# Kernel optimization log

Measured on AMD Instinct MI355X. Metric: run time of the kernel, lower is better.

The kernel has to match this reference:

```python
import jax, jax.numpy as jnp
import numpy as np

N_NODES = 50000
N_EDGES = 25000
NNZ = 800000
IN_DIM = 256
OUT_DIM = 256


def setup_inputs() -> dict:
    key = jax.random.key(0)
    k1, k2, k3, k4, k5 = jax.random.split(key, 5)
    X = jax.random.normal(k1, (N_NODES, IN_DIM), dtype=jnp.float32)
    node_idx = jax.random.randint(k2, (NNZ,), 0, N_NODES, dtype=jnp.int64)
    edge_idx = jax.random.randint(k3, (NNZ,), 0, N_EDGES, dtype=jnp.int64)
    # Xavier-uniform-ish weight, zero bias (matches reset_parameters)
    limit = float(np.sqrt(6.0 / (IN_DIM + OUT_DIM)))
    W = jax.random.uniform(k4, (IN_DIM, OUT_DIM), dtype=jnp.float32, minval=-limit, maxval=limit)
    b = jnp.zeros((OUT_DIM,), dtype=jnp.float32)
    return {"X": X, "node_idx": node_idx, "edge_idx": edge_idx, "W": W, "b": b}


def reference(X, node_idx, edge_idx, W, b):
    # Y = X @ W + b  -- dense GEMM
    Y = X @ W + b  # [N, out_dim]

    ones = jnp.ones(node_idx.shape[0], dtype=Y.dtype)
    # D_v = rowsum(H)^-0.5 (inf -> 0); D_e = colsum(H)^-1 (inf -> 0)
    deg_v = jax.ops.segment_sum(ones, node_idx, num_segments=N_NODES)
    deg_e = jax.ops.segment_sum(ones, edge_idx, num_segments=N_EDGES)
    d_v = jnp.where(deg_v > 0, deg_v ** -0.5, 0.0)  # [N]
    d_e = jnp.where(deg_e > 0, 1.0 / deg_e, 0.0)    # [E]

    # step1 = H^T @ (D_v X): gather scaled node rows, scatter-add into edges
    Z = d_v[:, None] * Y                                   # [N, out_dim]
    step1 = jax.ops.segment_sum(Z[node_idx], edge_idx, num_segments=N_EDGES)  # [E, out_dim]
    # step2 = D_e @ step1
    step2 = d_e[:, None] * step1                           # [E, out_dim]
    # step3 = H @ step2: gather edge rows, scatter-add into nodes
    step3 = jax.ops.segment_sum(step2[edge_idx], node_idx, num_segments=N_NODES)  # [N, out_dim]
    # final = D_v @ step3
    return d_v[:, None] * step3
```

## Files before the change

kernel.cpp:

```cpp
#include <hip/hip_runtime.h>

#define N_NODES 50000
#define N_EDGES 25000
#define NNZ     800000
#define DIM     256

#define CAP_E 88
#define CAP_V 56

#define NBE 98
#define NBV 196
#define CE_COARSE 8800
#define CV_COARSE 4500
#define NNZ_PB 2048
#define P1_BLOCKS 391

#define B_A1   0
#define B_CE   0
#define B_CV   3449600
#define B_CSRE 12800000
#define B_CSRV 17200000
#define B_WT   22800000
#define B_CURV 22931072
#define B_CURE 23131072
#define B_CCUR 23331072
#define B_DV   23332248

typedef __attribute__((ext_vector_type(8))) short s8v;
typedef __attribute__((ext_vector_type(4))) float f4v;

__device__ __forceinline__ unsigned short f2bf(float f) {
    unsigned u = __float_as_uint(f);
    u = (u + 0x7FFFu + ((u >> 16) & 1u)) >> 16;
    return (unsigned short)u;
}
__device__ __forceinline__ float bf2f(unsigned short h) {
    return __uint_as_float(((unsigned)h) << 16);
}

__global__ __launch_bounds__(256) void k_prep(
        const float* __restrict__ W,
        const int* __restrict__ node_idx, const int* __restrict__ edge_idx,
        unsigned short* __restrict__ WTb,
        unsigned* __restrict__ ccurE, unsigned* __restrict__ ccurV,
        unsigned* __restrict__ coarseE, unsigned* __restrict__ coarseV) {
    if (blockIdx.x < 32) {
        int t = blockIdx.x * 256 + threadIdx.x;
        int n = t >> 5;
        int k0 = (t & 31) * 8;
        unsigned short o[8];
#pragma unroll
        for (int j = 0; j < 8; ++j) o[j] = f2bf(W[(size_t)(k0 + j) * DIM + n]);
        *(s8v*)(WTb + (size_t)n * DIM + k0) = *(const s8v*)o;
        return;
    }

    __shared__ unsigned histE[NBE], histV[NBV], baseE[NBE], baseV[NBV];
    __shared__ unsigned offE[NBE], offV[NBV];
    __shared__ unsigned scanE[256], scanV[256];
    __shared__ unsigned nEs, nVs;
    __shared__ unsigned bufE[NNZ_PB], dstE[NNZ_PB];
    __shared__ unsigned bufV[NNZ_PB], dstV[NNZ_PB];
    const int tid = threadIdx.x;
    const int pb  = blockIdx.x - 32;
    const int base = pb * NNZ_PB;

    if (tid < NBE) histE[tid] = 0;
    if (tid < NBV) histV[tid] = 0;
    __syncthreads();

    int idx0 = base + tid * 4;
    int idx1 = base + 1024 + tid * 4;
    bool ok0 = idx0 < NNZ, ok1 = idx1 < NNZ;
    int4 v0 = ok0 ? *(const int4*)(node_idx + idx0) : (int4){0,0,0,0};
    int4 e0 = ok0 ? *(const int4*)(edge_idx + idx0) : (int4){0,0,0,0};
    int4 v1 = ok1 ? *(const int4*)(node_idx + idx1) : (int4){0,0,0,0};
    int4 e1 = ok1 ? *(const int4*)(edge_idx + idx1) : (int4){0,0,0,0};
    int vv[8] = {v0.x, v0.y, v0.z, v0.w, v1.x, v1.y, v1.z, v1.w};
    int ee[8] = {e0.x, e0.y, e0.z, e0.w, e1.x, e1.y, e1.z, e1.w};

    unsigned short locE[8], locV[8];
#pragma unroll
    for (int j = 0; j < 8; ++j) {
        bool ok = (j < 4) ? ok0 : ok1;
        if (ok) {
            locE[j] = (unsigned short)atomicAdd(&histE[ee[j] >> 8], 1u);
            locV[j] = (unsigned short)atomicAdd(&histV[vv[j] >> 8], 1u);
        }
    }
    __syncthreads();
    if (tid < NBE) baseE[tid] = atomicAdd(&ccurE[tid], histE[tid]);
    if (tid < NBV) baseV[tid] = atomicAdd(&ccurV[tid], histV[tid]);
    scanE[tid] = (tid < NBE) ? histE[tid] : 0u;
    scanV[tid] = (tid < NBV) ? histV[tid] : 0u;
    __syncthreads();
    for (int off = 1; off < 256; off <<= 1) {
        unsigned tE = (tid >= off) ? scanE[tid - off] : 0u;
        unsigned tV = (tid >= off) ? scanV[tid - off] : 0u;
        __syncthreads();
        scanE[tid] += tE;
        scanV[tid] += tV;
        __syncthreads();
    }
    if (tid < NBE) offE[tid] = scanE[tid] - histE[tid];
    if (tid < NBV) offV[tid] = scanV[tid] - histV[tid];
    if (tid == 0) { nEs = scanE[255]; nVs = scanV[255]; }
    __syncthreads();

#pragma unroll
    for (int j = 0; j < 8; ++j) {
        bool ok = (j < 4) ? ok0 : ok1;
        if (ok) {
            unsigned e = (unsigned)ee[j], v = (unsigned)vv[j];
            unsigned be = e >> 8, bv = v >> 8;
            unsigned se = offE[be] + locE[j];
            unsigned pe = baseE[be] + locE[j];
            bufE[se] = ((e & 255u) << 16) | v;
            dstE[se] = (pe < CE_COARSE) ? (be * CE_COARSE + pe) : 0xFFFFFFFFu;
            unsigned sv = offV[bv] + locV[j];
            unsigned pv = baseV[bv] + locV[j];
            bufV[sv] = ((v & 255u) << 16) | e;
            dstV[sv] = (pv < CV_COARSE) ? (bv * CV_COARSE + pv) : 0xFFFFFFFFu;
        }
    }
    __syncthreads();

    unsigned nE = nEs, nV = nVs;
    for (unsigned i = tid; i < nE; i += 256) {
        unsigned d = dstE[i];
        if (d != 0xFFFFFFFFu) coarseE[d] = bufE[i];
    }
    for (unsigned i = tid; i < nV; i += 256) {
        unsigned d = dstV[i];
        if (d != 0xFFFFFFFFu) coarseV[d] = bufV[i];
    }
}

__global__ __launch_bounds__(1024) void k_fine(
        const unsigned* __restrict__ coarseE, const unsigned* __restrict__ coarseV,
        const unsigned* __restrict__ ccurE, const unsigned* __restrict__ ccurV,
        unsigned short* __restrict__ csrE, unsigned short* __restrict__ csrV,
        unsigned* __restrict__ cur_e, unsigned* __restrict__ cur_v,
        float* __restrict__ dv) {
    __shared__ unsigned cnt[256];
    __shared__ __align__(16) unsigned short slots[256 * CAP_E];
    const int tid = threadIdx.x;
    if (tid < 256) cnt[tid] = 0;
    __syncthreads();

    if (blockIdx.x < NBE) {
        int b = blockIdx.x;
        unsigned n = ccurE[b]; n = n < CE_COARSE ? n : CE_COARSE;
        const unsigned* src = coarseE + (size_t)b * CE_COARSE;
        for (unsigned i = tid; i < n; i += 1024) {
            unsigned p = src[i];
            unsigned f = p >> 16, v = p & 0xFFFFu;
            unsigned pos = atomicAdd(&cnt[f], 1u);
            if (pos < CAP_E) slots[f * CAP_E + pos] = (unsigned short)v;
        }
        __syncthreads();
        if (tid < 256) {
            int e = b * 256 + tid;
            if (e < N_EDGES) cur_e[e] = cnt[tid];
        }
        int rows = N_EDGES - b * 256; rows = rows < 256 ? rows : 256;
        unsigned q4 = (unsigned)rows * (CAP_E / 2) / 4;
        uint4* dst = (uint4*)(csrE + (size_t)b * 256 * CAP_E);
        const uint4* s = (const uint4*)slots;
        for (unsigned i = tid; i < q4; i += 1024) dst[i] = s[i];
    } else {
        int b = blockIdx.x - NBE;
        unsigned n = ccurV[b]; n = n < CV_COARSE ? n : CV_COARSE;
        const unsigned* src = coarseV + (size_t)b * CV_COARSE;
        for (unsigned i = tid; i < n; i += 1024) {
            unsigned p = src[i];
            unsigned f = p >> 16, e = p & 0xFFFFu;
            unsigned pos = atomicAdd(&cnt[f], 1u);
            if (pos < CAP_V) slots[f * CAP_V + pos] = (unsigned short)e;
        }
        __syncthreads();
        if (tid < 256) {
            int v = b * 256 + tid;
            if (v < N_NODES) {
                unsigned c = cnt[tid];
                cur_v[v] = c;
                dv[v] = c ? __frsqrt_rn((float)c) : 0.0f;
            }
        }
        int rows = N_NODES - b * 256; rows = rows < 256 ? rows : 256;
        unsigned q4 = (unsigned)rows * (CAP_V / 2) / 4;
        uint4* dst = (uint4*)(csrV + (size_t)b * 256 * CAP_V);
        const uint4* s = (const uint4*)slots;
        for (unsigned i = tid; i < q4; i += 1024) dst[i] = s[i];
    }
}

__global__ __launch_bounds__(256) void k_gemm_y(
        const float* __restrict__ X,
        const unsigned short* __restrict__ WT,
        const float* __restrict__ bias,
        unsigned short* __restrict__ Yb) {
    __shared__ unsigned short As[64][264];
    const int tid  = threadIdx.x;
    const int wv   = tid >> 6;
    const int lane = tid & 63;
    const int quad = lane >> 4;
    const int l16  = lane & 15;
    const int r0   = blockIdx.x * 64;
    const int nb   = wv * 64;

#pragma unroll
    for (int it = 0; it < 16; ++it) {
        int i   = tid + it * 256;
        int row = i >> 6;
        int c4  = i & 63;
        int src = r0 + row;
        src = (src < N_NODES) ? src : (N_NODES - 1);
        float4 p = *(const float4*)(X + (size_t)src * DIM + c4 * 4);
        unsigned short o[4] = {f2bf(p.x), f2bf(p.y), f2bf(p.z), f2bf(p.w)};
        *(ushort4*)(&As[row][c4 * 4]) = *(const ushort4*)o;
    }
    __syncthreads();

    f4v acc[4][4];
#pragma unroll
    for (int mt = 0; mt < 4; ++mt)
#pragma unroll
        for (int nt = 0; nt < 4; ++nt) acc[mt][nt] = (f4v){0.f, 0.f, 0.f, 0.f};

    for (int k0 = 0; k0 < DIM; k0 += 32) {
        s8v a[4], b[4];
#pragma unroll
        for (int nt = 0; nt < 4; ++nt) {
            int n = nb + nt * 16 + l16;
            b[nt] = *(const s8v*)(WT + (size_t)n * DIM + k0 + quad * 8);
        }
#pragma unroll
        for (int mt = 0; mt < 4; ++mt)
            a[mt] = *(const s8v*)(&As[mt * 16 + l16][k0 + quad * 8]);
#pragma unroll
        for (int mt = 0; mt < 4; ++mt)
#pragma unroll
            for (int nt = 0; nt < 4; ++nt)
                acc[mt][nt] = __builtin_amdgcn_mfma_f32_16x16x32_bf16(
                    a[mt], b[nt], acc[mt][nt], 0, 0, 0);
    }

    float bv[4];
#pragma unroll
    for (int nt = 0; nt < 4; ++nt) bv[nt] = bias[nb + nt * 16 + l16];

#pragma unroll
    for (int mt = 0; mt < 4; ++mt) {
#pragma unroll
        for (int reg = 0; reg < 4; ++reg) {
            int row = r0 + mt * 16 + quad * 4 + reg;
            if (row < N_NODES) {
#pragma unroll
                for (int nt = 0; nt < 4; ++nt) {
                    Yb[(size_t)row * DIM + nb + nt * 16 + l16] =
                        f2bf(acc[mt][nt][reg] + bv[nt]);
                }
            }
        }
    }
}

__global__ __launch_bounds__(256) void k_gather_edges(
        const unsigned short* __restrict__ Yb,
        const unsigned short* __restrict__ csrE,
        const unsigned* __restrict__ cur_e,
        const float* __restrict__ dv,
        unsigned short* __restrict__ S2) {
    int w = (blockIdx.x * 256 + threadIdx.x) >> 6;
    int lane = threadIdx.x & 63;
    if (w >= N_EDGES) return;
    unsigned deg = cur_e[w];
    unsigned cnt = deg < CAP_E ? deg : CAP_E;
    float sc = deg ? 1.0f / (float)deg : 0.0f;
    const unsigned short* lst = csrE + (size_t)w * CAP_E;
    unsigned idp = (lane < CAP_E / 2) ? ((const unsigned*)lst)[lane] : 0u;
    const unsigned short* xb = Yb + (size_t)lane * 4;

    float ax = 0.f, ay = 0.f, az = 0.f, aw = 0.f;

#define EFETCH(J, X0, X1, X2, X3, S0, S1, S2_, S3)                         \
    {                                                                      \
        unsigned p0 = __shfl(idp, (int)((J) >> 1));                        \
        unsigned p1 = __shfl(idp, (int)((J) >> 1) + 1);                    \
        unsigned v0 = p0 & 0xFFFFu, v1 = p0 >> 16;                         \
        unsigned v2 = p1 & 0xFFFFu, v3 = p1 >> 16;                         \
        S0 = dv[v0]; S1 = dv[v1]; S2_ = dv[v2]; S3 = dv[v3];               \
        X0 = *(const ushort4*)(xb + ((size_t)v0 << 8));                    \
        X1 = *(const ushort4*)(xb + ((size_t)v1 << 8));                    \
        X2 = *(const ushort4*)(xb + ((size_t)v2 << 8));                    \
        X3 = *(const ushort4*)(xb + ((size_t)v3 << 8));                    \
    }
#define ECONS(X0, X1, X2, X3, S0, S1, S2_, S3)                             \
    {                                                                      \
        ax = fmaf(S0, bf2f(X0.x), ax); ay = fmaf(S0, bf2f(X0.y), ay);      \
        az = fmaf(S0, bf2f(X0.z), az); aw = fmaf(S0, bf2f(X0.w), aw);      \
        ax = fmaf(S1, bf2f(X1.x), ax); ay = fmaf(S1, bf2f(X1.y), ay);      \
        az = fmaf(S1, bf2f(X1.z), az); aw = fmaf(S1, bf2f(X1.w), aw);      \
        ax = fmaf(S2_, bf2f(X2.x), ax); ay = fmaf(S2_, bf2f(X2.y), ay);    \
        az = fmaf(S2_, bf2f(X2.z), az); aw = fmaf(S2_, bf2f(X2.w), aw);    \
        ax = fmaf(S3, bf2f(X3.x), ax); ay = fmaf(S3, bf2f(X3.y), ay);      \
        az = fmaf(S3, bf2f(X3.z), az); aw = fmaf(S3, bf2f(X3.w), aw);      \
    }

    unsigned quads = cnt >> 2;
    unsigned j = 0;
    if (quads) {
        ushort4 a0, a1, a2, a3, b0, b1, b2, b3;
        float r0, r1, r2, r3, t0, t1, t2, t3;
        EFETCH(0u, a0, a1, a2, a3, r0, r1, r2, r3);
        unsigned q = 1;
        for (; q + 1 < quads; q += 2) {
            EFETCH(4u * q,      b0, b1, b2, b3, t0, t1, t2, t3);
            ECONS(a0, a1, a2, a3, r0, r1, r2, r3);
            EFETCH(4u * q + 4u, a0, a1, a2, a3, r0, r1, r2, r3);
            ECONS(b0, b1, b2, b3, t0, t1, t2, t3);
        }
        if (q < quads) {
            EFETCH(4u * q, b0, b1, b2, b3, t0, t1, t2, t3);
            ECONS(a0, a1, a2, a3, r0, r1, r2, r3);
            ECONS(b0, b1, b2, b3, t0, t1, t2, t3);
        } else {
            ECONS(a0, a1, a2, a3, r0, r1, r2, r3);
        }
        j = quads << 2;
    }
    for (; j < cnt; ++j) {
        unsigned p = __shfl(idp, (int)(j >> 1));
        unsigned v = (j & 1) ? (p >> 16) : (p & 0xFFFFu);
        float s = dv[v];
        ushort4 x = *(const ushort4*)(xb + ((size_t)v << 8));
        ax = fmaf(s, bf2f(x.x), ax); ay = fmaf(s, bf2f(x.y), ay);
        az = fmaf(s, bf2f(x.z), az); aw = fmaf(s, bf2f(x.w), aw);
    }
#undef EFETCH
#undef ECONS

    ushort4 o = {f2bf(sc * ax), f2bf(sc * ay), f2bf(sc * az), f2bf(sc * aw)};
    *(ushort4*)(S2 + (size_t)w * DIM + lane * 4) = o;
}

__global__ __launch_bounds__(256) void k_gather_nodes(
        const unsigned short* __restrict__ S2,
        const unsigned short* __restrict__ csrV,
        const unsigned* __restrict__ cur_v,
        const float* __restrict__ dv,
        float* __restrict__ out) {
    int w = (blockIdx.x * 256 + threadIdx.x) >> 6;
    int lane = threadIdx.x & 63;
    if (w >= N_NODES) return;
    unsigned cnt = cur_v[w]; cnt = cnt < CAP_V ? cnt : CAP_V;
    const unsigned short* lst = csrV + (size_t)w * CAP_V;
    unsigned idp = (lane < CAP_V / 2) ? ((const unsigned*)lst)[lane] : 0u;
    const unsigned short* sb = S2 + (size_t)lane * 4;

    float ax = 0.f, ay = 0.f, az = 0.f, aw = 0.f;

#define NFETCH(J, X0, X1, X2, X3)                                          \
    {                                                                      \
        unsigned p0 = __shfl(idp, (int)((J) >> 1));                        \
        unsigned p1 = __shfl(idp, (int)((J) >> 1) + 1);                    \
        unsigned e0 = p0 & 0xFFFFu, e1 = p0 >> 16;                         \
        unsigned e2 = p1 & 0xFFFFu, e3 = p1 >> 16;                         \
        X0 = *(const ushort4*)(sb + ((size_t)e0 << 8));                    \
        X1 = *(const ushort4*)(sb + ((size_t)e1 << 8));                    \
        X2 = *(const ushort4*)(sb + ((size_t)e2 << 8));                    \
        X3 = *(const ushort4*)(sb + ((size_t)e3 << 8));                    \
    }
#define NCONS(X0, X1, X2, X3)                                              \
    {                                                                      \
        ax += (bf2f(X0.x) + bf2f(X1.x)) + (bf2f(X2.x) + bf2f(X3.x));       \
        ay += (bf2f(X0.y) + bf2f(X1.y)) + (bf2f(X2.y) + bf2f(X3.y));       \
        az += (bf2f(X0.z) + bf2f(X1.z)) + (bf2f(X2.z) + bf2f(X3.z));       \
        aw += (bf2f(X0.w) + bf2f(X1.w)) + (bf2f(X2.w) + bf2f(X3.w));       \
    }

    unsigned quads = cnt >> 2;
    unsigned j = 0;
    if (quads) {
        ushort4 a0, a1, a2, a3, b0, b1, b2, b3;
        NFETCH(0u, a0, a1, a2, a3);
        unsigned q = 1;
        for (; q + 1 < quads; q += 2) {
            NFETCH(4u * q,      b0, b1, b2, b3);
            NCONS(a0, a1, a2, a3);
            NFETCH(4u * q + 4u, a0, a1, a2, a3);
            NCONS(b0, b1, b2, b3);
        }
        if (q < quads) {
            NFETCH(4u * q, b0, b1, b2, b3);
            NCONS(a0, a1, a2, a3);
            NCONS(b0, b1, b2, b3);
        } else {
            NCONS(a0, a1, a2, a3);
        }
        j = quads << 2;
    }
    for (; j < cnt; ++j) {
        unsigned p = __shfl(idp, (int)(j >> 1));
        unsigned e = (j & 1) ? (p >> 16) : (p & 0xFFFFu);
        ushort4 x = *(const ushort4*)(sb + ((size_t)e << 8));
        ax += bf2f(x.x); ay += bf2f(x.y); az += bf2f(x.z); aw += bf2f(x.w);
    }
#undef NFETCH
#undef NCONS

    float s = dv[w];
    float4 o = {s * ax, s * ay, s * az, s * aw};
    *(float4*)(out + (size_t)w * DIM + lane * 4) = o;
}

extern "C" void kernel_launch(void* const* d_in, const int* in_sizes, int n_in,
                              void* d_out, int out_size, void* d_ws, size_t ws_size,
                              hipStream_t stream) {
    (void)in_sizes; (void)n_in; (void)out_size; (void)ws_size;
    const float* X        = (const float*)d_in[0];
    const int*   node_idx = (const int*)d_in[1];
    const int*   edge_idx = (const int*)d_in[2];
    const float* W        = (const float*)d_in[3];
    const float* bias     = (const float*)d_in[4];
    float* out = (float*)d_out;
    char*  ws  = (char*)d_ws;

    unsigned short* S2      = (unsigned short*)(ws + B_A1);
    unsigned*       coarseE = (unsigned*)(ws + B_CE);
    unsigned*       coarseV = (unsigned*)(ws + B_CV);
    unsigned short* csrE    = (unsigned short*)(ws + B_CSRE);
    unsigned short* csrV    = (unsigned short*)(ws + B_CSRV);
    unsigned short* WTb     = (unsigned short*)(ws + B_WT);
    unsigned*       cur_v   = (unsigned*)(ws + B_CURV);
    unsigned*       cur_e   = (unsigned*)(ws + B_CURE);
    unsigned*       ccurE   = (unsigned*)(ws + B_CCUR);
    unsigned*       ccurV   = ccurE + NBE;
    float*          dv      = (float*)(ws + B_DV);

    unsigned short* Yb = (unsigned short*)d_out;

    (void)hipMemsetAsync(ccurE, 0, (NBE + NBV) * sizeof(unsigned), stream);

    k_prep<<<32 + P1_BLOCKS, 256, 0, stream>>>(W, node_idx, edge_idx,
                                               WTb, ccurE, ccurV, coarseE, coarseV);
    k_fine<<<NBE + NBV, 1024, 0, stream>>>(coarseE, coarseV, ccurE, ccurV,
                                           csrE, csrV, cur_e, cur_v, dv);
    k_gemm_y<<<(N_NODES + 63) / 64, 256, 0, stream>>>(X, WTb, bias, Yb);
    k_gather_edges<<<(N_EDGES * 64 + 255) / 256, 256, 0, stream>>>(
        Yb, csrE, cur_e, dv, S2);
    k_gather_nodes<<<(N_NODES * 64 + 255) / 256, 256, 0, stream>>>(
        S2, csrV, cur_v, dv, out);
}
```

Measured before the change: 248.6 us.

## Fuse dense GEMM with coarse bucketing into one launch for overlap

Splits the W transpose/bf16 conversion into its own small kernel and merges the GEMM blocks with the coarse CSR bucketing blocks into one combined launch that uses a shared union smem buffer. The compute-heavy GEMM and the atomic/scatter-heavy bucketing now run concurrently instead of in separate serialized kernels. The aim is to overlap the two and cut a launch boundary. The cost is that the combined kernel's shared-memory footprint is set by the larger branch, and one extra tiny kernel launch is added.

```diff
diff --git a/kernel.cpp b/kernel.cpp
--- a/kernel.cpp
+++ b/kernel.cpp
@@ -14,6 +14,7 @@
 #define CV_COARSE 4500
 #define NNZ_PB 2048
 #define P1_BLOCKS 391
+#define GEMM_BLOCKS 782
 
 #define B_A1   0
 #define B_CE   0
@@ -38,31 +39,110 @@
     return __uint_as_float(((unsigned)h) << 16);
 }
 
-__global__ __launch_bounds__(256) void k_prep(
-        const float* __restrict__ W,
+__global__ __launch_bounds__(256) void k_wt(
+        const float* __restrict__ W, unsigned short* __restrict__ WTb) {
+    int t = blockIdx.x * 256 + threadIdx.x;
+    int n = t >> 5;
+    int k0 = (t & 31) * 8;
+    unsigned short o[8];
+#pragma unroll
+    for (int j = 0; j < 8; ++j) o[j] = f2bf(W[(size_t)(k0 + j) * DIM + n]);
+    *(s8v*)(WTb + (size_t)n * DIM + k0) = *(const s8v*)o;
+}
+
+__global__ __launch_bounds__(256) void k_bg(
+        const float* __restrict__ X,
+        const unsigned short* __restrict__ WT,
+        const float* __restrict__ bias,
+        unsigned short* __restrict__ Yb,
         const int* __restrict__ node_idx, const int* __restrict__ edge_idx,
-        unsigned short* __restrict__ WTb,
         unsigned* __restrict__ ccurE, unsigned* __restrict__ ccurV,
         unsigned* __restrict__ coarseE, unsigned* __restrict__ coarseV) {
-    if (blockIdx.x < 32) {
-        int t = blockIdx.x * 256 + threadIdx.x;
-        int n = t >> 5;
-        int k0 = (t & 31) * 8;
-        unsigned short o[8];
-#pragma unroll
-        for (int j = 0; j < 8; ++j) o[j] = f2bf(W[(size_t)(k0 + j) * DIM + n]);
-        *(s8v*)(WTb + (size_t)n * DIM + k0) = *(const s8v*)o;
+    __shared__ __align__(16) char smem[39424];
+    const int tid = threadIdx.x;
+
+    if (blockIdx.x < GEMM_BLOCKS) {
+        unsigned short (*As)[264] = (unsigned short (*)[264])smem;
+        const int wv   = tid >> 6;
+        const int lane = tid & 63;
+        const int quad = lane >> 4;
+        const int l16  = lane & 15;
+        const int r0   = blockIdx.x * 64;
+        const int nb   = wv * 64;
+
+#pragma unroll
+        for (int it = 0; it < 16; ++it) {
+            int i   = tid + it * 256;
+            int row = i >> 6;
+            int c4  = i & 63;
+            int src = r0 + row;
+            src = (src < N_NODES) ? src : (N_NODES - 1);
+            float4 p = *(const float4*)(X + (size_t)src * DIM + c4 * 4);
+            unsigned short o[4] = {f2bf(p.x), f2bf(p.y), f2bf(p.z), f2bf(p.w)};
+            *(ushort4*)(&As[row][c4 * 4]) = *(const ushort4*)o;
+        }
+        __syncthreads();
+
+        f4v acc[4][4];
+#pragma unroll
+        for (int mt = 0; mt < 4; ++mt)
+#pragma unroll
+            for (int nt = 0; nt < 4; ++nt) acc[mt][nt] = (f4v){0.f, 0.f, 0.f, 0.f};
+
+        for (int k0 = 0; k0 < DIM; k0 += 32) {
+            s8v a[4], b[4];
+#pragma unroll
+            for (int nt = 0; nt < 4; ++nt) {
+                int n = nb + nt * 16 + l16;
+                b[nt] = *(const s8v*)(WT + (size_t)n * DIM + k0 + quad * 8);
+            }
+#pragma unroll
+            for (int mt = 0; mt < 4; ++mt)
+                a[mt] = *(const s8v*)(&As[mt * 16 + l16][k0 + quad * 8]);
+#pragma unroll
+            for (int mt = 0; mt < 4; ++mt)
+#pragma unroll
+                for (int nt = 0; nt < 4; ++nt)
+                    acc[mt][nt] = __builtin_amdgcn_mfma_f32_16x16x32_bf16(
+                        a[mt], b[nt], acc[mt][nt], 0, 0, 0);
+        }
+
+        float bv[4];
+#pragma unroll
+        for (int nt = 0; nt < 4; ++nt) bv[nt] = bias[nb + nt * 16 + l16];
+
+#pragma unroll
+        for (int mt = 0; mt < 4; ++mt) {
+#pragma unroll
+            for (int reg = 0; reg < 4; ++reg) {
+                int row = r0 + mt * 16 + quad * 4 + reg;
+                if (row < N_NODES) {
+#pragma unroll
+                    for (int nt = 0; nt < 4; ++nt) {
+                        Yb[(size_t)row * DIM + nb + nt * 16 + l16] =
+                            f2bf(acc[mt][nt][reg] + bv[nt]);
+                    }
+                }
+            }
+        }
         return;
     }
 
-    __shared__ unsigned histE[NBE], histV[NBV], baseE[NBE], baseV[NBV];
-    __shared__ unsigned offE[NBE], offV[NBV];
-    __shared__ unsigned scanE[256], scanV[256];
-    __shared__ unsigned nEs, nVs;
-    __shared__ unsigned bufE[NNZ_PB], dstE[NNZ_PB];
-    __shared__ unsigned bufV[NNZ_PB], dstV[NNZ_PB];
-    const int tid = threadIdx.x;
-    const int pb  = blockIdx.x - 32;
+    unsigned* histE = (unsigned*)smem;
+    unsigned* histV = histE + NBE;
+    unsigned* baseE = histV + NBV;
+    unsigned* baseV = baseE + NBE;
+    unsigned* offE  = baseV + NBV;
+    unsigned* offV  = offE + NBE;
+    unsigned* scanE = offV + NBV;
+    unsigned* scanV = scanE + 256;
+    unsigned* nn    = scanV + 256;
+    unsigned* bufE  = nn + 2;
+    unsigned* dstE  = bufE + NNZ_PB;
+    unsigned* bufV  = dstE + NNZ_PB;
+    unsigned* dstV  = bufV + NNZ_PB;
+
+    const int pb  = blockIdx.x - GEMM_BLOCKS;
     const int base = pb * NNZ_PB;
 
     if (tid < NBE) histE[tid] = 0;
@@ -104,7 +184,7 @@
     }
     if (tid < NBE) offE[tid] = scanE[tid] - histE[tid];
     if (tid < NBV) offV[tid] = scanV[tid] - histV[tid];
-    if (tid == 0) { nEs = scanE[255]; nVs = scanV[255]; }
+    if (tid == 0) { nn[0] = scanE[255]; nn[1] = scanV[255]; }
     __syncthreads();
 
 #pragma unroll
@@ -125,7 +205,7 @@
     }
     __syncthreads();
 
-    unsigned nE = nEs, nV = nVs;
+    unsigned nE = nn[0], nV = nn[1];
     for (unsigned i = tid; i < nE; i += 256) {
         unsigned d = dstE[i];
         if (d != 0xFFFFFFFFu) coarseE[d] = bufE[i];
@@ -192,77 +272,6 @@
         uint4* dst = (uint4*)(csrV + (size_t)b * 256 * CAP_V);
         const uint4* s = (const uint4*)slots;
         for (unsigned i = tid; i < q4; i += 1024) dst[i] = s[i];
-    }
-}
-
-__global__ __launch_bounds__(256) void k_gemm_y(
-        const float* __restrict__ X,
-        const unsigned short* __restrict__ WT,
-        const float* __restrict__ bias,
-        unsigned short* __restrict__ Yb) {
-    __shared__ unsigned short As[64][264];
-    const int tid  = threadIdx.x;
-    const int wv   = tid >> 6;
-    const int lane = tid & 63;
-    const int quad = lane >> 4;
-    const int l16  = lane & 15;
-    const int r0   = blockIdx.x * 64;
-    const int nb   = wv * 64;
-
-#pragma unroll
-    for (int it = 0; it < 16; ++it) {
-        int i   = tid + it * 256;
-        int row = i >> 6;
-        int c4  = i & 63;
-        int src = r0 + row;
-        src = (src < N_NODES) ? src : (N_NODES - 1);
-        float4 p = *(const float4*)(X + (size_t)src * DIM + c4 * 4);
-        unsigned short o[4] = {f2bf(p.x), f2bf(p.y), f2bf(p.z), f2bf(p.w)};
-        *(ushort4*)(&As[row][c4 * 4]) = *(const ushort4*)o;
-    }
-    __syncthreads();
-
-    f4v acc[4][4];
-#pragma unroll
-    for (int mt = 0; mt < 4; ++mt)
-#pragma unroll
-        for (int nt = 0; nt < 4; ++nt) acc[mt][nt] = (f4v){0.f, 0.f, 0.f, 0.f};
-
-    for (int k0 = 0; k0 < DIM; k0 += 32) {
-        s8v a[4], b[4];
-#pragma unroll
-        for (int nt = 0; nt < 4; ++nt) {
-            int n = nb + nt * 16 + l16;
-            b[nt] = *(const s8v*)(WT + (size_t)n * DIM + k0 + quad * 8);
-        }
-#pragma unroll
-        for (int mt = 0; mt < 4; ++mt)
-            a[mt] = *(const s8v*)(&As[mt * 16 + l16][k0 + quad * 8]);
-#pragma unroll
-        for (int mt = 0; mt < 4; ++mt)
-#pragma unroll
-            for (int nt = 0; nt < 4; ++nt)
-                acc[mt][nt] = __builtin_amdgcn_mfma_f32_16x16x32_bf16(
-                    a[mt], b[nt], acc[mt][nt], 0, 0, 0);
-    }
-
-    float bv[4];
-#pragma unroll
-    for (int nt = 0; nt < 4; ++nt) bv[nt] = bias[nb + nt * 16 + l16];
-
-#pragma unroll
-    for (int mt = 0; mt < 4; ++mt) {
-#pragma unroll
-        for (int reg = 0; reg < 4; ++reg) {
-            int row = r0 + mt * 16 + quad * 4 + reg;
-            if (row < N_NODES) {
-#pragma unroll
-                for (int nt = 0; nt < 4; ++nt) {
-                    Yb[(size_t)row * DIM + nb + nt * 16 + l16] =
-                        f2bf(acc[mt][nt][reg] + bv[nt]);
-                }
-            }
-        }
     }
 }
 
@@ -443,11 +452,11 @@
 
     (void)hipMemsetAsync(ccurE, 0, (NBE + NBV) * sizeof(unsigned), stream);
 
-    k_prep<<<32 + P1_BLOCKS, 256, 0, stream>>>(W, node_idx, edge_idx,
-                                               WTb, ccurE, ccurV, coarseE, coarseV);
+    k_wt<<<32, 256, 0, stream>>>(W, WTb);
+    k_bg<<<GEMM_BLOCKS + P1_BLOCKS, 256, 0, stream>>>(
+        X, WTb, bias, Yb, node_idx, edge_idx, ccurE, ccurV, coarseE, coarseV);
     k_fine<<<NBE + NBV, 1024, 0, stream>>>(coarseE, coarseV, ccurE, ccurV,
                                            csrE, csrV, cur_e, cur_v, dv);
-    k_gemm_y<<<(N_NODES + 63) / 64, 256, 0, stream>>>(X, WTb, bias, Yb);
     k_gather_edges<<<(N_EDGES * 64 + 255) / 256, 256, 0, stream>>>(
         Yb, csrE, cur_e, dv, S2);
     k_gather_nodes<<<(N_NODES * 64 + 255) / 256, 256, 0, stream>>>(
```

Result: faster. 241.7 us (-2.8%).
